# Optimization experiments

Hardware: AMD Instinct MI355X
Metric: run time of the kernel (lower is better)

The kernel has to match this reference:

```python
import jax, jax.numpy as jnp
import numpy as np

B, SP, SH, H = 32, 256, 256, 512
D = 2 * H       # input feature dim (2*hidden_size)
E = H // 2      # per-liner output dim
FD = 4 * H      # fusion linear dim
EPS = 1e-13


def setup_inputs() -> dict:
    key = jax.random.key(0)
    ks = jax.random.split(key, 8)
    s = 0.02
    return dict(
        premise_batch=jax.random.normal(ks[0], (B, SP, D), jnp.float32),
        hypothesis_batch=jax.random.normal(ks[1], (B, SH, D), jnp.float32),
        premise_mask=jax.random.randint(ks[2], (B, SP), 0, 2).astype(jnp.int32),
        hypothesis_mask=jax.random.randint(ks[3], (B, SH), 0, 2).astype(jnp.int32),
        W8=jax.random.normal(ks[4], (8, D, E), jnp.float32) * s,   # liner1..8 weights (in,out)
        B8=jnp.zeros((8, E), jnp.float32),
        Wl=jax.random.normal(ks[5], (8 * E, FD), jnp.float32) * s,  # self.liner
        bl=jnp.zeros((FD,), jnp.float32),
        Wp=jax.random.normal(ks[6], (7 * D, H), jnp.float32) * s,   # self._projection
        bp=jnp.zeros((H,), jnp.float32),
    )


def masked_softmax(logits, mask):
    # ESIM-style: multiply logits by mask, softmax, re-mask, renormalize.
    m = mask[:, None, :]                        # (b,1,kv)
    r = jax.nn.softmax(logits * m, axis=-1) * m
    return r / (r.sum(axis=-1, keepdims=True) + EPS)


def fuse(x, imp_self, imp_inter, W8, B8, Wl, bl):
    # x: (b,s,D); imp_*: (b,s,1). Eight modulated views -> liner1..8 -> concat -> liner+ReLU.
    a1 = imp_self * imp_inter
    a2 = imp_self + imp_inter
    a3 = jnp.maximum(imp_self, imp_inter)
    x1 = x * imp_self
    x2 = x * imp_inter
    mx = jnp.maximum(x1, x2)
    feats = jnp.stack([x * a1, x * a2, x * a3, mx,
                       x * (a1 + 1.0), x * (a2 + 1.0), x * (a3 + 1.0), mx + x], 0)  # (8,b,s,D)
    h = jnp.einsum('kbsd,kde->kbse', feats, W8) + B8[:, None, None, :]              # (8,b,s,E)
    cat = jnp.moveaxis(h, 0, 2).reshape(x.shape[0], x.shape[1], 8 * E)              # concat order 1..8
    return jax.nn.relu(cat @ Wl + bl)           # dropout is identity in eval mode


def reference(premise_batch, hypothesis_batch, premise_mask, hypothesis_mask,
              W8, B8, Wl, bl, Wp, bp):
    pm = premise_mask.astype(jnp.float32)
    hm = hypothesis_mask.astype(jnp.float32)
    scale = 1.0 / jnp.sqrt(jnp.float32(premise_batch.shape[-1]))

    sim = jnp.einsum('bpd,bhd->bph', premise_batch, hypothesis_batch) * scale
    ph = masked_softmax(sim, hm)                               # (b,Sp,Sh)
    hp = masked_softmax(sim.transpose(0, 2, 1), pm)            # (b,Sh,Sp)
    att_p = jnp.einsum('bph,bhd->bpd', ph, hypothesis_batch) * pm[:, :, None]
    att_h = jnp.einsum('bhp,bpd->bhd', hp, premise_batch) * hm[:, :, None]

    sp_attn = jax.nn.softmax(jnp.einsum('bpd,bqd->bpq', premise_batch, premise_batch) * scale, axis=-1)
    sh_attn = jax.nn.softmax(jnp.einsum('bpd,bqd->bpq', hypothesis_batch, hypothesis_batch) * scale, axis=-1)
    self_p = sp_attn @ premise_batch
    self_h = sh_attn @ hypothesis_batch

    imp_p = sp_attn.sum(axis=-2)[..., None]        # (b,Sp,1)
    imp_h = sh_attn.sum(axis=-2)[..., None]        # (b,Sh,1)
    inter_imp_h = ph.sum(axis=-2)[..., None]       # (b,Sh,1)
    inter_imp_p = hp.sum(axis=-2)[..., None]       # (b,Sp,1)

    p_all = fuse(premise_batch, imp_p, inter_imp_p, W8, B8, Wl, bl)
    h_all = fuse(hypothesis_batch, imp_h, inter_imp_h, W8, B8, Wl, bl)

    enh_p = jnp.concatenate([premise_batch, att_p, self_p, p_all,
                             premise_batch * att_p, premise_batch - att_p], axis=-1)
    enh_h = jnp.concatenate([hypothesis_batch, att_h, self_h, h_all,
                             hypothesis_batch * att_h, hypothesis_batch - att_h], axis=-1)
    out_p = jax.nn.relu(enh_p @ Wp + bp)
    out_h = jax.nn.relu(enh_h @ Wp + bp)
    return out_p, out_h
```

## Files before the change

### kernel.cpp

```cpp
#include <hip/hip_runtime.h>
#include <hip/hip_bf16.h>
#include <cmath>

#define BB 32
#define SS 256
#define DD 1024
#define EE 256
#define FDIM 2048
#define HH 512
#define KOUT6 (6 * 1024)
#define NROW (BB * SS)
#define NROW2 (2 * NROW)
#define SIMSZ ((size_t)BB * SS * SS)

static constexpr float SCALE = 1.0f / 32.0f;
static constexpr float EPSF  = 1e-13f;

typedef __attribute__((ext_vector_type(8))) short bf16x8;
typedef __attribute__((ext_vector_type(4))) float f32x4;

__device__ inline float4 ld4(const float* p) { return *(const float4*)p; }
__device__ inline ushort f2b(float f) {
    uint x = __float_as_uint(f);
    x += 0x7fffu + ((x >> 16) & 1u);
    return (ushort)(x >> 16);
}
__device__ inline float b2f(ushort u) { return __uint_as_float(((uint)u) << 16); }
__device__ inline bf16x8 cvt8(const float* v) {
    bf16x8 r;
#pragma unroll
    for (int j = 0; j < 8; ++j) r[j] = (short)f2b(v[j]);
    return r;
}
__device__ inline void b2f8(bf16x8 v, float* o) {
#pragma unroll
    for (int j = 0; j < 8; ++j) o[j] = b2f((ushort)v[j]);
}
__device__ inline bf16x8 ldf8(const float* p) {
    const float4 u0 = ld4(p), u1 = ld4(p + 4);
    float v[8] = {u0.x, u0.y, u0.z, u0.w, u1.x, u1.y, u1.z, u1.w};
    return cvt8(v);
}

typedef __attribute__((address_space(1))) const uchar gas_t;
typedef __attribute__((address_space(3))) uchar las_t;
__device__ inline void gll16(const ushort* g, ushort* l) {
    __builtin_amdgcn_global_load_lds((gas_t*)g, (las_t*)l, 16, 0, 0);
}

__device__ inline int swz_orig_2d() {
    const int n   = blockIdx.y * gridDim.x + blockIdx.x;
    const int tot = gridDim.x * gridDim.y;
    return (n & 7) * (tot >> 3) + (n >> 3);
}
__device__ inline int swz_orig_3d() {
    const int n   = (blockIdx.z * gridDim.y + blockIdx.y) * gridDim.x + blockIdx.x;
    const int tot = gridDim.x * gridDim.y * gridDim.z;
    return (n & 7) * (tot >> 3) + (n >> 3);
}

__global__ __launch_bounds__(256)
void tpose_cvt_k(const float* __restrict__ in, ushort* __restrict__ out,
                 int K, int N, size_t inStride, size_t outStride) {
    __shared__ float T[32][33];
    const float* ib = in  + (size_t)blockIdx.z * inStride;
    ushort*      ob = out + (size_t)blockIdx.z * outStride;
    const int k0 = blockIdx.x * 32, n0 = blockIdx.y * 32;
    const int tx = threadIdx.x & 31, ty = threadIdx.x >> 5;
#pragma unroll
    for (int i = 0; i < 4; ++i) T[ty + 8 * i][tx] = ib[(size_t)(k0 + ty + 8 * i) * N + n0 + tx];
    __syncthreads();
#pragma unroll
    for (int i = 0; i < 4; ++i)
        ob[(size_t)(n0 + ty + 8 * i) * K + k0 + tx] = f2b(T[tx][ty + 8 * i]);
}

__global__ __launch_bounds__(256)
void tpose_wp_k(const float* __restrict__ Wp, ushort* __restrict__ out) {
    __shared__ float T[32][33];
    const int k0 = blockIdx.x * 32, n0 = blockIdx.y * 32;
    const int tx = threadIdx.x & 31, ty = threadIdx.x >> 5;
#pragma unroll
    for (int i = 0; i < 4; ++i) {
        const int k = k0 + ty + 8 * i, n = n0 + tx;
        float v = Wp[(size_t)k * HH + n];
        if (k < DD)           v += Wp[(size_t)(k + 6 * DD) * HH + n];
        else if (k < 2 * DD)  v -= Wp[(size_t)(k + 5 * DD) * HH + n];
        T[ty + 8 * i][tx] = v;
    }
    __syncthreads();
#pragma unroll
    for (int i = 0; i < 4; ++i)
        out[(size_t)(n0 + ty + 8 * i) * KOUT6 + k0 + tx] = f2b(T[tx][ty + 8 * i]);
}

__global__ __launch_bounds__(256)
void prep_xprod_k(const float* __restrict__ P, const float* __restrict__ H,
                  const ushort* __restrict__ attAb,
                  ushort* __restrict__ Xb, ushort* __restrict__ prodb) {
    const int idx = blockIdx.x * 256 + threadIdx.x;
    const int row = idx >> 7, chunk = idx & 127;
    const size_t off = (size_t)row * DD + chunk * 8;
    const float* X = (row < NROW) ? (P + off) : (H + off - (size_t)NROW * DD);
    const float4 x0 = ld4(X), x1 = ld4(X + 4);
    float xv[8] = {x0.x, x0.y, x0.z, x0.w, x1.x, x1.y, x1.z, x1.w};
    float av[8];
    b2f8(*(const bf16x8*)&attAb[off], av);
    float pv[8];
#pragma unroll
    for (int j = 0; j < 8; ++j) pv[j] = xv[j] * av[j];
    *(bf16x8*)&Xb[off]    = cvt8(xv);
    *(bf16x8*)&prodb[off] = cvt8(pv);
}

__global__ __launch_bounds__(256)
void reduce_out_k(float* __restrict__ out, const float* __restrict__ p1,
                  const float* __restrict__ bp) {
    const int gid = blockIdx.x * 256 + threadIdx.x;
    const size_t o = (size_t)gid * 4;
    const float4 a = ld4(&out[o]);
    const float4 b = ld4(&p1[o]);
    const float4 bv = ld4(&bp[(int)(o & 511)]);
    *(float4*)&out[o] = make_float4(fmaxf(a.x + b.x + bv.x, 0.f),
                                    fmaxf(a.y + b.y + bv.y, 0.f),
                                    fmaxf(a.z + b.z + bv.z, 0.f),
                                    fmaxf(a.w + b.w + bv.w, 0.f));
}

__global__ __launch_bounds__(256)
void softmax4_k(ushort* __restrict__ simPH, ushort* __restrict__ simPHT,
                ushort* __restrict__ simPP, ushort* __restrict__ simHH,
                const int* __restrict__ pma, const int* __restrict__ hma) {
    const int job = blockIdx.y;
    ushort* buf = job == 0 ? simPH : job == 1 ? simPHT : job == 2 ? simPP : simHH;
    const int* mask = job == 0 ? hma : job == 1 ? pma : nullptr;
    const int w = threadIdx.x >> 6, lane = threadIdx.x & 63;
    const int row = blockIdx.x * 4 + w;
    const int b = row >> 8;
    ushort* rp = buf + (size_t)row * SS + lane * 4;
    ushort4 u = *(const ushort4*)rp;
    float z[4], mj[4];
    const ushort uv[4] = {u.x, u.y, u.z, u.w};
#pragma unroll
    for (int c = 0; c < 4; ++c) {
        const float v = b2f(uv[c]);
        float m = 1.f;
        if (mask) m = (float)mask[b * SS + lane * 4 + c];
        mj[c] = m; z[c] = v * m;
    }
    float M = fmaxf(fmaxf(z[0], z[1]), fmaxf(z[2], z[3]));
#pragma unroll
    for (int off = 1; off < 64; off <<= 1) M = fmaxf(M, __shfl_xor(M, off));
    float e[4], r[4], sz = 0.f, sr = 0.f;
#pragma unroll
    for (int c = 0; c < 4; ++c) {
        e[c] = expf(z[c] - M);
        r[c] = e[c] * mj[c];
        sz += e[c]; sr += r[c];
    }
#pragma unroll
    for (int off = 1; off < 64; off <<= 1) {
        sz += __shfl_xor(sz, off);
        sr += __shfl_xor(sr, off);
    }
    ushort4 o;
    if (mask) {
        const float d = 1.f / (sr + EPSF * sz);
        o.x = f2b(r[0] * d); o.y = f2b(r[1] * d); o.z = f2b(r[2] * d); o.w = f2b(r[3] * d);
    } else {
        const float d = 1.f / sz;
        o.x = f2b(e[0] * d); o.y = f2b(e[1] * d); o.z = f2b(e[2] * d); o.w = f2b(e[3] * d);
    }
    *(ushort4*)rp = o;
}

__global__ __launch_bounds__(256)
void colsum_p1_k(const ushort* __restrict__ simPP, const ushort* __restrict__ simHH,
                 const ushort* __restrict__ simPHT, const ushort* __restrict__ simPH,
                 float* __restrict__ pbuf) {
    const int job = blockIdx.y, b = blockIdx.x, rc = blockIdx.z, j = threadIdx.x;
    const ushort* src = job == 0 ? simPP : job == 1 ? simHH : job == 2 ? simPHT : simPH;
    const ushort* Mb = src + (size_t)b * SS * SS + (size_t)rc * 32 * SS;
    float s = 0.f;
#pragma unroll 4
    for (int i = 0; i < 32; ++i) s += b2f(Mb[i * SS + j]);
    pbuf[(((size_t)job * BB + b) * 8 + rc) * SS + j] = s;
}

__global__ __launch_bounds__(256)
void colsum_p2_k(const float* __restrict__ pbuf,
                 float* __restrict__ impS, float* __restrict__ impI) {
    const int job = blockIdx.y, b = blockIdx.x, j = threadIdx.x;
    const float* pb = pbuf + ((size_t)job * BB + b) * 8 * SS;
    float s = 0.f;
#pragma unroll
    for (int rc = 0; rc < 8; ++rc) s += pb[rc * SS + j];
    float* dst = job == 0 ? impS : job == 1 ? impS + NROW : job == 2 ? impI : impI + NROW;
    dst[b * SS + j] = s;
}

#define LSWZ(kg, r) ((r) ^ ((kg) << 1))
#define FRAG_R(T, r) (*(const bf16x8*)T[kq][LSWZ(kq, r)])
#define FRAG_G(T, r) (*(const bf16x8*)&T[r][(kq ^ ((r) & 3)) * 8])

#define MFMA_TAIL(afr, bfr)                                                          \
    _Pragma("unroll") for (int m = 0; m < 4; ++m)                                    \
        _Pragma("unroll") for (int n = 0; n < 4; ++n)                                \
            acc[m][n] = __builtin_amdgcn_mfma_f32_16x16x32_bf16(                     \
                afr[m], bfr[n], acc[m][n], 0, 0, 0);

#define MFMA_CORE_R()                                                                \
    {                                                                                \
        bf16x8 afr[4], bfr[4];                                                       \
        _Pragma("unroll") for (int m = 0; m < 4; ++m) afr[m] = FRAG_R(As, wr + m * 16 + fr); \
        _Pragma("unroll") for (int n = 0; n < 4; ++n) bfr[n] = FRAG_R(Bs, wc + n * 16 + fr); \
        MFMA_TAIL(afr, bfr)                                                          \
    }

#define MFMA_CORE_G()                                                                \
    {                                                                                \
        bf16x8 afr[4], bfr[4];                                                       \
        _Pragma("unroll") for (int m = 0; m < 4; ++m) afr[m] = FRAG_G(As, wr + m * 16 + fr); \
        _Pragma("unroll") for (int n = 0; n < 4; ++n) bfr[n] = FRAG_G(Bs, wc + n * 16 + fr); \
        MFMA_TAIL(afr, bfr)                                                          \
    }

#define MFMA_CORE_RG()                                                               \
    {                                                                                \
        bf16x8 afr[4], bfr[4];                                                       \
        _Pragma("unroll") for (int m = 0; m < 4; ++m) afr[m] = FRAG_R(As, wr + m * 16 + fr); \
        _Pragma("unroll") for (int n = 0; n < 4; ++n) bfr[n] = FRAG_G(Bs, wc + n * 16 + fr); \
        MFMA_TAIL(afr, bfr)                                                          \
    }

#define MFMA_PREAMBLE()                                                              \
    const int tid = threadIdx.x;                                                     \
    const int lane = tid & 63;                                                       \
    const int w = tid >> 6;                                                          \
    const int wr = (w >> 1) * 64, wc = (w & 1) * 64;                                 \
    const int fr = lane & 15;                                                        \
    const int kq = lane >> 4;                                                        \
    const int rq = kq * 4;                                                           \
    f32x4 acc[4][4] = {};

#define GLL_STAGE2(seg, pitch, r0, kloc, T)                                          \
    {                                                                                \
        const int rl0_ = w * 32 + (lane >> 2);                                       \
        const int cp_ = lane & 3;                                                    \
        gll16((seg) + (size_t)((r0) + rl0_) * (pitch) + (kloc) + ((cp_ ^ (rl0_ & 3)) * 8), \
              &T[w * 32][0]);                                                        \
        const int rl1_ = rl0_ + 16;                                                  \
        gll16((seg) + (size_t)((r0) + rl1_) * (pitch) + (kloc) + ((cp_ ^ (rl1_ & 3)) * 8), \
              &T[w * 32 + 16][0]);                                                   \
    }

__global__ __launch_bounds__(256)
void mfma_nt_k(const float* __restrict__ P, const float* __restrict__ H,
               ushort* __restrict__ simPH, ushort* __restrict__ simPHT,
               ushort* __restrict__ simPP, ushort* __restrict__ simHH) {
    __shared__ __align__(16) ushort As[4][128][8];
    __shared__ __align__(16) ushort Bs[4][128][8];
    int orig = swz_orig_3d();
    const int cb = orig & 1; orig >>= 1;
    const int rb = orig & 1; orig >>= 1;
    const int g = orig >> 5, b = orig & 31;
    const float* Au = ((g == 2) ? H : P) + (size_t)b * SS * DD;
    const float* Bu = ((g == 1) ? P : H) + (size_t)b * SS * DD;
    const int col0 = cb * 128, row0 = rb * 128;
    MFMA_PREAMBLE();
    for (int k0 = 0; k0 < DD; k0 += 32) {
        bf16x8 ar[2], br[2];
#pragma unroll
        for (int i = 0; i < 2; ++i) {
            const int cid = tid + i * 256, srow = cid >> 2, skc = (cid & 3) * 8;
            ar[i] = ldf8(&Au[(size_t)(row0 + srow) * DD + k0 + skc]);
            br[i] = ldf8(&Bu[(size_t)(col0 + srow) * DD + k0 + skc]);
        }
        __syncthreads();
#pragma unroll
        for (int i = 0; i < 2; ++i) {
            const int cid = tid + i * 256, kg = cid & 3, rr = LSWZ(kg, cid >> 2);
            *(bf16x8*)As[kg][rr] = ar[i];
            *(bf16x8*)Bs[kg][rr] = br[i];
        }
        __syncthreads();
        MFMA_CORE_R();
    }
    ushort* Cb = (g == 0 ? simPH : g == 1 ? simPP : simHH) + (size_t)b * SS * SS;
#pragma unroll
    for (int m = 0; m < 4; ++m)
#pragma unroll
        for (int n = 0; n < 4; ++n) {
            const int c = col0 + wc + n * 16 + fr;
            const int r0 = row0 + wr + m * 16 + rq;
#pragma unroll
            for (int r = 0; r < 4; ++r) Cb[(size_t)(r0 + r) * SS + c] = f2b(acc[m][n][r] * SCALE);
            if (g == 0) {
                ushort* Tb = simPHT + (size_t)b * SS * SS;
                ushort4 t;
                t.x = f2b(acc[m][n][0] * SCALE); t.y = f2b(acc[m][n][1] * SCALE);
                t.z = f2b(acc[m][n][2] * SCALE); t.w = f2b(acc[m][n][3] * SCALE);
                *(ushort4*)&Tb[(size_t)c * SS + r0] = t;
            }
        }
}

__global__ __launch_bounds__(256)
void mfma_att_k(const ushort* __restrict__ ph, const ushort* __restrict__ hp,
                const ushort* __restrict__ spA, const ushort* __restrict__ shA,
                const ushort* __restrict__ PbT, const ushort* __restrict__ HbT,
                const int* __restrict__ pma, const int* __restrict__ hma,
                ushort* __restrict__ attAb, ushort* __restrict__ selfAb) {
    __shared__ __align__(16) ushort As[128][32];
    __shared__ __align__(16) ushort Bs[128][32];
    int orig = swz_orig_3d();
    const int x = orig & 7; orig >>= 3;
    const int y = orig & 1; orig >>= 1;
    const int g = orig >> 5, b = orig & 31;
    const ushort* W  = (g == 0 ? ph : g == 1 ? hp : g == 2 ? spA : shA) + (size_t)b * SS * SS;
    const ushort* BT = ((g == 0 || g == 3) ? HbT : PbT) + (size_t)b * DD * SS;
    const int* rmask = g == 0 ? pma + b * SS : g == 1 ? hma + b * SS : nullptr;
    const int side = (g == 1 || g == 3);
    ushort* Ob = (g < 2 ? attAb : selfAb) + ((size_t)side * NROW + (size_t)b * SS) * DD;
    const int col0 = x * 128, row0 = y * 128;
    MFMA_PREAMBLE();
    for (int k0 = 0; k0 < SS; k0 += 32) {
        __syncthreads();
        GLL_STAGE2(W,  SS, row0, k0, As);
        GLL_STAGE2(BT, SS, col0, k0, Bs);
        __syncthreads();
        MFMA_CORE_G();
    }
#pragma unroll
    for (int m = 0; m < 4; ++m)
#pragma unroll
        for (int n = 0; n < 4; ++n) {
            const int c = col0 + wc + n * 16 + fr;
#pragma unroll
            for (int r = 0; r < 4; ++r) {
                const int rr = row0 + wr + m * 16 + rq + r;
                const float mm = rmask ? (float)rmask[rr] : 1.0f;
                Ob[(size_t)rr * DD + c] = f2b(acc[m][n][r] * mm);
            }
        }
}

__global__ __launch_bounds__(256)
void mfma_fuse_k(const float* __restrict__ P, const float* __restrict__ H,
                 const float* __restrict__ impS, const float* __restrict__ impI,
                 const ushort* __restrict__ W8T, const float* __restrict__ B8v,
                 ushort* __restrict__ catb) {
    __shared__ __align__(16) ushort As[4][128][8];
    __shared__ __align__(16) ushort Bs[128][32];
    const int orig = swz_orig_2d();
    const int cb = orig & 15, rb = orig >> 4;
    const int kf = cb >> 1, e0 = (cb & 1) * 128, row0 = rb * 128;
    const float* X = (row0 < NROW) ? P : H;
    const int rbase = (row0 < NROW) ? row0 : row0 - NROW;
    MFMA_PREAMBLE();
    const ushort* Wk = W8T + (size_t)kf * EE * DD;

    int srow_[2]; float sA[2], iA[2], cf[2];
#pragma unroll
    for (int i = 0; i < 2; ++i) {
        const int cid = tid + i * 256;
        srow_[i] = cid >> 2;
        const float s_ = impS[row0 + srow_[i]], i_ = impI[row0 + srow_[i]];
        sA[i] = s_; iA[i] = i_;
        float c = 0.f;
        switch (kf) {
            case 0: c = s_ * i_;             break;
            case 1: c = s_ + i_;             break;
            case 2: c = fmaxf(s_, i_);       break;
            case 4: c = s_ * i_ + 1.f;       break;
            case 5: c = s_ + i_ + 1.f;       break;
            case 6: c = fmaxf(s_, i_) + 1.f; break;
            default: break;
        }
        cf[i] = c;
    }
    for (int k0 = 0; k0 < DD; k0 += 32) {
        bf16x8 ar[2];
#pragma unroll
        for (int i = 0; i < 2; ++i) {
            const int cid = tid + i * 256, skc = (cid & 3) * 8;
            const float* src = &X[(size_t)(rbase + srow_[i]) * DD + k0 + skc];
            const float4 u0 = ld4(src), u1 = ld4(src + 4);
            float v[8] = {u0.x, u0.y, u0.z, u0.w, u1.x, u1.y, u1.z, u1.w};
            if (kf == 3) {
#pragma unroll
                for (int j = 0; j < 8; ++j) v[j] = fmaxf(v[j] * sA[i], v[j] * iA[i]);
            } else if (kf == 7) {
#pragma unroll
                for (int j = 0; j < 8; ++j) v[j] = fmaxf(v[j] * sA[i], v[j] * iA[i]) + v[j];
            } else {
#pragma unroll
                for (int j = 0; j < 8; ++j) v[j] *= cf[i];
            }
            ar[i] = cvt8(v);
        }
        __syncthreads();
        GLL_STAGE2(Wk, DD, e0, k0, Bs);
#pragma unroll
        for (int i = 0; i < 2; ++i) {
            const int cid = tid + i * 256, kg = cid & 3, rr = LSWZ(kg, cid >> 2);
            *(bf16x8*)As[kg][rr] = ar[i];
        }
        __syncthreads();
        MFMA_CORE_RG();
    }
#pragma unroll
    for (int m = 0; m < 4; ++m)
#pragma unroll
        for (int n = 0; n < 4; ++n) {
            const int el = e0 + wc + n * 16 + fr;
            const float bv = B8v[kf * EE + el];
#pragma unroll
            for (int r = 0; r < 4; ++r) {
                const int rr = row0 + wr + m * 16 + rq + r;
                catb[(size_t)rr * FDIM + kf * EE + el] = f2b(acc[m][n][r] + bv);
            }
        }
}

__global__ __launch_bounds__(256)
void mfma_lin_k(const ushort* __restrict__ A, const ushort* __restrict__ BT,
                const float* __restrict__ bias, ushort* __restrict__ C) {
    __shared__ __align__(16) ushort As[128][32];
    __shared__ __align__(16) ushort Bs[128][32];
    const int orig = swz_orig_2d();
    const int col0 = (orig & 15) * 128, row0 = (orig >> 4) * 128;
    MFMA_PREAMBLE();
    for (int k0 = 0; k0 < FDIM; k0 += 32) {
        __syncthreads();
        GLL_STAGE2(A,  FDIM, row0, k0, As);
        GLL_STAGE2(BT, FDIM, col0, k0, Bs);
        __syncthreads();
        MFMA_CORE_G();
    }
#pragma unroll
    for (int m = 0; m < 4; ++m)
#pragma unroll
        for (int n = 0; n < 4; ++n) {
            const int c = col0 + wc + n * 16 + fr;
            const float bv = bias[c];
#pragma unroll
            for (int r = 0; r < 4; ++r) {
                const int rr = row0 + wr + m * 16 + rq + r;
                C[(size_t)rr * FDIM + c] = f2b(fmaxf(acc[m][n][r] + bv, 0.f));
            }
        }
}

__device__ inline void out_seg(int k0, const ushort* Xb, const ushort* attAb,
                               const ushort* selfAb, const ushort* pallb,
                               const ushort* prodb,
                               const ushort*& seg, int& pitch, int& kloc) {
    switch (k0 >> 10) {
        case 0:  seg = Xb;     pitch = DD;   kloc = k0;          break;
        case 1:  seg = attAb;  pitch = DD;   kloc = k0 - DD;     break;
        case 2:  seg = selfAb; pitch = DD;   kloc = k0 - 2 * DD; break;
        case 3:
        case 4:  seg = pallb;  pitch = FDIM; kloc = k0 - 3 * DD; break;
        default: seg = prodb;  pitch = DD;   kloc = k0 - 5 * DD; break;
    }
}

__global__ __launch_bounds__(256)
void mfma_out_k(const ushort* __restrict__ Xb, const ushort* __restrict__ attAb,
                const ushort* __restrict__ selfAb, const ushort* __restrict__ pallb,
                const ushort* __restrict__ prodb, const ushort* __restrict__ WpT,
                const float* __restrict__ bp, float* __restrict__ dst0,
                float* __restrict__ dst1, int kchunk, int finalize) {
    __shared__ __align__(16) ushort As[128][32];
    __shared__ __align__(16) ushort Bs[128][32];
    int orig = swz_orig_3d();
    const int x = orig & 3; orig >>= 2;
    const int y = orig & 127; orig >>= 7;
    const int z = orig;
    const int col0 = x * 128, row0 = y * 128;
    const int kbase = z * kchunk;
    float* dst = z == 0 ? dst0 : dst1;
    MFMA_PREAMBLE();
    for (int t = 0; t < kchunk / 32; ++t) {
        const int k0 = kbase + t * 32;
        const ushort* seg; int pitch, kloc;
        out_seg(k0, Xb, attAb, selfAb, pallb, prodb, seg, pitch, kloc);
        __syncthreads();
        GLL_STAGE2(seg, pitch, row0, kloc, As);
        GLL_STAGE2(WpT, KOUT6, col0, k0, Bs);
        __syncthreads();
        MFMA_CORE_G();
    }
#pragma unroll
    for (int m = 0; m < 4; ++m)
#pragma unroll
        for (int n = 0; n < 4; ++n) {
            const int c = col0 + wc + n * 16 + fr;
            const float bv = finalize ? bp[c] : 0.f;
#pragma unroll
            for (int r = 0; r < 4; ++r) {
                const int rr = row0 + wr + m * 16 + rq + r;
                const float v = acc[m][n][r] + bv;
                dst[(size_t)rr * HH + c] = finalize ? fmaxf(v, 0.f) : v;
            }
        }
}

extern "C" void kernel_launch(void* const* d_in, const int* in_sizes, int n_in,
                              void* d_out, int out_size, void* d_ws, size_t ws_size,
                              hipStream_t stream) {
    const float* P   = (const float*)d_in[0];
    const float* Hb  = (const float*)d_in[1];
    const int*   pma = (const int*)d_in[2];
    const int*   hma = (const int*)d_in[3];
    const float* W8  = (const float*)d_in[4];
    const float* B8v = (const float*)d_in[5];
    const float* Wl  = (const float*)d_in[6];
    const float* bl  = (const float*)d_in[7];
    const float* Wp  = (const float*)d_in[8];
    const float* bp  = (const float*)d_in[9];

    char* base = (char*)d_ws;
    ushort* simPH  = (ushort*)base;
    ushort* simPHT = simPH  + SIMSZ;
    ushort* simPP  = simPHT + SIMSZ;
    ushort* simHH  = simPP  + SIMSZ;
    ushort* PbT    = simHH + SIMSZ;
    ushort* HbT    = PbT + (size_t)NROW * DD;
    ushort* catb   = (ushort*)base;
    ushort* Xb     = (ushort*)base;
    ushort* prodb  = Xb + (size_t)NROW2 * DD;
    char* cur = base + (size_t)NROW2 * FDIM * 2;
    auto alloc_f = [&](size_t n) { float*  p = (float*)cur;  cur += n * 4; return p; };
    auto alloc_u = [&](size_t n) { ushort* p = (ushort*)cur; cur += n * 2; return p; };
    float*  impS   = alloc_f(NROW2);
    float*  impI   = alloc_f(NROW2);
    ushort* attAb  = alloc_u((size_t)NROW2 * DD);
    ushort* selfAb = alloc_u((size_t)NROW2 * DD);
    ushort* pallb  = alloc_u((size_t)NROW2 * FDIM);
    ushort* WlT    = alloc_u((size_t)FDIM * FDIM);
    ushort* WpT    = alloc_u((size_t)HH * KOUT6);
    ushort* W8T    = alloc_u((size_t)8 * EE * DD);
    float*  pbuf   = alloc_f((size_t)4 * BB * 8 * SS);
    float*  part1  = alloc_f((size_t)NROW2 * HH);

    const size_t need_split = (size_t)((char*)(part1 + (size_t)NROW2 * HH) - base);
    const bool split = ws_size >= need_split;

    float* outp = (float*)d_out;
    const dim3 blk(256);

    tpose_cvt_k<<<dim3(8, 32, BB), blk, 0, stream>>>(P,  PbT, SS, DD, (size_t)SS * DD, (size_t)DD * SS);
    tpose_cvt_k<<<dim3(8, 32, BB), blk, 0, stream>>>(Hb, HbT, SS, DD, (size_t)SS * DD, (size_t)DD * SS);
    tpose_cvt_k<<<dim3(FDIM / 32, FDIM / 32, 1), blk, 0, stream>>>(Wl, WlT, FDIM, FDIM, 0, 0);
    tpose_wp_k<<<dim3(KOUT6 / 32, HH / 32, 1), blk, 0, stream>>>(Wp, WpT);
    tpose_cvt_k<<<dim3(DD / 32, EE / 32, 8), blk, 0, stream>>>(W8, W8T, DD, EE,
                                                               (size_t)DD * EE, (size_t)EE * DD);

    mfma_nt_k<<<dim3(2, 2, 96), blk, 0, stream>>>(P, Hb, simPH, simPHT, simPP, simHH);
    softmax4_k<<<dim3(NROW / 4, 4), blk, 0, stream>>>(simPH, simPHT, simPP, simHH, pma, hma);
    colsum_p1_k<<<dim3(BB, 4, 8), blk, 0, stream>>>(simPP, simHH, simPHT, simPH, pbuf);
    colsum_p2_k<<<dim3(BB, 4), blk, 0, stream>>>(pbuf, impS, impI);
    mfma_att_k<<<dim3(8, 2, 128), blk, 0, stream>>>(simPH, simPHT, simPP, simHH, PbT, HbT,
                                                    pma, hma, attAb, selfAb);

    mfma_fuse_k<<<dim3(16, 128), blk, 0, stream>>>(P, Hb, impS, impI, W8T, B8v, catb);
    mfma_lin_k<<<dim3(16, 128), blk, 0, stream>>>(catb, WlT, bl, pallb);
    prep_xprod_k<<<dim3(NROW2 * DD / 8 / 256), blk, 0, stream>>>(P, Hb, attAb, Xb, prodb);
    if (split) {
        mfma_out_k<<<dim3(4, 128, 2), blk, 0, stream>>>(Xb, attAb, selfAb, pallb, prodb,
                                                        WpT, bp, outp, part1, KOUT6 / 2, 0);
        reduce_out_k<<<dim3(NROW2 * HH / 4 / 256), blk, 0, stream>>>(outp, part1, bp);
    } else {
        mfma_out_k<<<dim3(4, 128, 1), blk, 0, stream>>>(Xb, attAb, selfAb, pallb, prodb,
                                                        WpT, bp, outp, outp, KOUT6, 1);
    }

    (void)in_sizes; (void)n_in; (void)out_size; (void)ws_size;
}
```

Baseline: 716.9 us.

## Factor per-row scale out of fuse GEMM and precompute bf16 inputs

Six of the eight modulated views are x times a per-row scalar, so the fuse GEMM now multiplies unscaled bf16 x by the weights and applies the coefficient in the epilogue. The two max-based views are rewritten as smin*x + (smax-smin)*relu(x), which needs a second accumulator fed by a sign-masked copy of x. A separate conversion kernel writes bf16 x once so the GEMM tiles can stream it with direct global-to-LDS loads. This trades an extra launch and an extra buffer pass against removing per-tile fp32 loads and elementwise scaling. It also changes rounding, since scaling now happens after the bf16 product, and it changes the LDS swizzle signature.

```diff
diff --git a/kernel.cpp b/kernel.cpp
--- a/kernel.cpp
+++ b/kernel.cpp
@@ -92,6 +92,18 @@
 #pragma unroll
     for (int i = 0; i < 4; ++i)
         out[(size_t)(n0 + ty + 8 * i) * KOUT6 + k0 + tx] = f2b(T[tx][ty + 8 * i]);
+}
+
+__global__ __launch_bounds__(256)
+void cvt_xb_k(const float* __restrict__ P, const float* __restrict__ H,
+              ushort* __restrict__ Xb) {
+    const int idx = blockIdx.x * 256 + threadIdx.x;
+    const int row = idx >> 7, chunk = idx & 127;
+    const size_t off = (size_t)row * DD + chunk * 8;
+    const float* X = (row < NROW) ? (P + off) : (H + off - (size_t)NROW * DD);
+    const float4 x0 = ld4(X), x1 = ld4(X + 4);
+    float xv[8] = {x0.x, x0.y, x0.z, x0.w, x1.x, x1.y, x1.z, x1.w};
+    *(bf16x8*)&Xb[off] = cvt8(xv);
 }
 
 __global__ __launch_bounds__(256)
@@ -200,21 +212,22 @@
 }
 
 #define LSWZ(kg, r) ((r) ^ ((kg) << 1))
+#define SIG(r) (((r) >> 1) & 3)
 #define FRAG_R(T, r) (*(const bf16x8*)T[kq][LSWZ(kq, r)])
-#define FRAG_G(T, r) (*(const bf16x8*)&T[r][(kq ^ ((r) & 3)) * 8])
-
-#define MFMA_TAIL(afr, bfr)                                                          \
+#define FRAG_G(T, r) (*(const bf16x8*)&T[r][(kq ^ SIG(r)) * 8])
+
+#define MFMA_TAIL(afr, bfr, ac)                                                      \
     _Pragma("unroll") for (int m = 0; m < 4; ++m)                                    \
         _Pragma("unroll") for (int n = 0; n < 4; ++n)                                \
-            acc[m][n] = __builtin_amdgcn_mfma_f32_16x16x32_bf16(                     \
-                afr[m], bfr[n], acc[m][n], 0, 0, 0);
+            ac[m][n] = __builtin_amdgcn_mfma_f32_16x16x32_bf16(                      \
+                afr[m], bfr[n], ac[m][n], 0, 0, 0);
 
 #define MFMA_CORE_R()                                                                \
     {                                                                                \
         bf16x8 afr[4], bfr[4];                                                       \
         _Pragma("unroll") for (int m = 0; m < 4; ++m) afr[m] = FRAG_R(As, wr + m * 16 + fr); \
         _Pragma("unroll") for (int n = 0; n < 4; ++n) bfr[n] = FRAG_R(Bs, wc + n * 16 + fr); \
-        MFMA_TAIL(afr, bfr)                                                          \
+        MFMA_TAIL(afr, bfr, acc)                                                     \
     }
 
 #define MFMA_CORE_G()                                                                \
@@ -222,15 +235,7 @@
         bf16x8 afr[4], bfr[4];                                                       \
         _Pragma("unroll") for (int m = 0; m < 4; ++m) afr[m] = FRAG_G(As, wr + m * 16 + fr); \
         _Pragma("unroll") for (int n = 0; n < 4; ++n) bfr[n] = FRAG_G(Bs, wc + n * 16 + fr); \
-        MFMA_TAIL(afr, bfr)                                                          \
-    }
-
-#define MFMA_CORE_RG()                                                               \
-    {                                                                                \
-        bf16x8 afr[4], bfr[4];                                                       \
-        _Pragma("unroll") for (int m = 0; m < 4; ++m) afr[m] = FRAG_R(As, wr + m * 16 + fr); \
-        _Pragma("unroll") for (int n = 0; n < 4; ++n) bfr[n] = FRAG_G(Bs, wc + n * 16 + fr); \
-        MFMA_TAIL(afr, bfr)                                                          \
+        MFMA_TAIL(afr, bfr, acc)                                                     \
     }
 
 #define MFMA_PREAMBLE()                                                              \
@@ -247,10 +252,10 @@
     {                                                                                \
         const int rl0_ = w * 32 + (lane >> 2);                                       \
         const int cp_ = lane & 3;                                                    \
-        gll16((seg) + (size_t)((r0) + rl0_) * (pitch) + (kloc) + ((cp_ ^ (rl0_ & 3)) * 8), \
+        gll16((seg) + (size_t)((r0) + rl0_) * (pitch) + (kloc) + ((cp_ ^ SIG(rl0_)) * 8), \
               &T[w * 32][0]);                                                        \
         const int rl1_ = rl0_ + 16;                                                  \
-        gll16((seg) + (size_t)((r0) + rl1_) * (pitch) + (kloc) + ((cp_ ^ (rl1_ & 3)) * 8), \
+        gll16((seg) + (size_t)((r0) + rl1_) * (pitch) + (kloc) + ((cp_ ^ SIG(rl1_)) * 8), \
               &T[w * 32 + 16][0]);                                                   \
     }
 
@@ -346,68 +351,24 @@
 }
 
 __global__ __launch_bounds__(256)
-void mfma_fuse_k(const float* __restrict__ P, const float* __restrict__ H,
-                 const float* __restrict__ impS, const float* __restrict__ impI,
-                 const ushort* __restrict__ W8T, const float* __restrict__ B8v,
-                 ushort* __restrict__ catb) {
-    __shared__ __align__(16) ushort As[4][128][8];
+void mfma_fuse_pure_k(const ushort* __restrict__ Xb, const float* __restrict__ impS,
+                      const float* __restrict__ impI, const ushort* __restrict__ W8T,
+                      const float* __restrict__ B8v, ushort* __restrict__ catb) {
+    __shared__ __align__(16) ushort As[128][32];
     __shared__ __align__(16) ushort Bs[128][32];
     const int orig = swz_orig_2d();
-    const int cb = orig & 15, rb = orig >> 4;
-    const int kf = cb >> 1, e0 = (cb & 1) * 128, row0 = rb * 128;
-    const float* X = (row0 < NROW) ? P : H;
-    const int rbase = (row0 < NROW) ? row0 : row0 - NROW;
+    const int cb = orig % 12, rb = orig / 12;
+    const int kidx = cb >> 1;
+    const int kf = kidx + (kidx >= 3 ? 1 : 0);
+    const int e0 = (cb & 1) * 128, row0 = rb * 128;
     MFMA_PREAMBLE();
     const ushort* Wk = W8T + (size_t)kf * EE * DD;
-
-    int srow_[2]; float sA[2], iA[2], cf[2];
-#pragma unroll
-    for (int i = 0; i < 2; ++i) {
-        const int cid = tid + i * 256;
-        srow_[i] = cid >> 2;
-        const float s_ = impS[row0 + srow_[i]], i_ = impI[row0 + srow_[i]];
-        sA[i] = s_; iA[i] = i_;
-        float c = 0.f;
-        switch (kf) {
-            case 0: c = s_ * i_;             break;
-            case 1: c = s_ + i_;             break;
-            case 2: c = fmaxf(s_, i_);       break;
-            case 4: c = s_ * i_ + 1.f;       break;
-            case 5: c = s_ + i_ + 1.f;       break;
-            case 6: c = fmaxf(s_, i_) + 1.f; break;
-            default: break;
-        }
-        cf[i] = c;
-    }
     for (int k0 = 0; k0 < DD; k0 += 32) {
-        bf16x8 ar[2];
-#pragma unroll
-        for (int i = 0; i < 2; ++i) {
-            const int cid = tid + i * 256, skc = (cid & 3) * 8;
-            const float* src = &X[(size_t)(rbase + srow_[i]) * DD + k0 + skc];
-            const float4 u0 = ld4(src), u1 = ld4(src + 4);
-            float v[8] = {u0.x, u0.y, u0.z, u0.w, u1.x, u1.y, u1.z, u1.w};
-            if (kf == 3) {
-#pragma unroll
-                for (int j = 0; j < 8; ++j) v[j] = fmaxf(v[j] * sA[i], v[j] * iA[i]);
-            } else if (kf == 7) {
-#pragma unroll
-                for (int j = 0; j < 8; ++j) v[j] = fmaxf(v[j] * sA[i], v[j] * iA[i]) + v[j];
-            } else {
-#pragma unroll
-                for (int j = 0; j < 8; ++j) v[j] *= cf[i];
-            }
-            ar[i] = cvt8(v);
-        }
-        __syncthreads();
+        __syncthreads();
+        GLL_STAGE2(Xb, DD, row0, k0, As);
         GLL_STAGE2(Wk, DD, e0, k0, Bs);
-#pragma unroll
-        for (int i = 0; i < 2; ++i) {
-            const int cid = tid + i * 256, kg = cid & 3, rr = LSWZ(kg, cid >> 2);
-            *(bf16x8*)As[kg][rr] = ar[i];
-        }
-        __syncthreads();
-        MFMA_CORE_RG();
+        __syncthreads();
+        MFMA_CORE_G();
     }
 #pragma unroll
     for (int m = 0; m < 4; ++m)
@@ -417,8 +378,84 @@
             const float bv = B8v[kf * EE + el];
 #pragma unroll
             for (int r = 0; r < 4; ++r) {
-                const int rr = row0 + wr + m * 16 + rq + r;
-                catb[(size_t)rr * FDIM + kf * EE + el] = f2b(acc[m][n][r] + bv);
+                const int row = row0 + wr + m * 16 + rq + r;
+                const float s_ = impS[row], i_ = impI[row];
+                float coef;
+                switch (kf) {
+                    case 0: coef = s_ * i_;             break;
+                    case 1: coef = s_ + i_;             break;
+                    case 2: coef = fmaxf(s_, i_);       break;
+                    case 4: coef = s_ * i_ + 1.f;       break;
+                    case 5: coef = s_ + i_ + 1.f;       break;
+                    default: coef = fmaxf(s_, i_) + 1.f; break;
+                }
+                catb[(size_t)row * FDIM + kf * EE + el] = f2b(coef * acc[m][n][r] + bv);
+            }
+        }
+}
+
+__global__ __launch_bounds__(256)
+void mfma_fuse_dual_k(const ushort* __restrict__ Xb, const float* __restrict__ impS,
+                      const float* __restrict__ impI, const ushort* __restrict__ W8T,
+                      const float* __restrict__ B8v, ushort* __restrict__ catb) {
+    __shared__ __align__(16) ushort AsX[4][128][8];
+    __shared__ __align__(16) ushort AsP[4][128][8];
+    __shared__ __align__(16) ushort Bs[128][32];
+    const int orig = swz_orig_2d();
+    const int cb = orig & 3, rb = orig >> 2;
+    const int kf = (cb >> 1) ? 7 : 3;
+    const int e0 = (cb & 1) * 128, row0 = rb * 128;
+    MFMA_PREAMBLE();
+    f32x4 accP[4][4] = {};
+    const ushort* Wk = W8T + (size_t)kf * EE * DD;
+    for (int k0 = 0; k0 < DD; k0 += 32) {
+        bf16x8 xr[2], pr[2];
+#pragma unroll
+        for (int i = 0; i < 2; ++i) {
+            const int cid = tid + i * 256, srow = cid >> 2, skc = (cid & 3) * 8;
+            xr[i] = *(const bf16x8*)&Xb[(size_t)(row0 + srow) * DD + k0 + skc];
+#pragma unroll
+            for (int j = 0; j < 8; ++j) {
+                const short s = xr[i][j];
+                pr[i][j] = (s & (short)0x8000) ? (short)0 : s;
+            }
+        }
+        __syncthreads();
+        GLL_STAGE2(Wk, DD, e0, k0, Bs);
+#pragma unroll
+        for (int i = 0; i < 2; ++i) {
+            const int cid = tid + i * 256, kg = cid & 3, rr = LSWZ(kg, cid >> 2);
+            *(bf16x8*)AsX[kg][rr] = xr[i];
+            *(bf16x8*)AsP[kg][rr] = pr[i];
+        }
+        __syncthreads();
+        {
+            bf16x8 ax[4], ap[4], bfr[4];
+#pragma unroll
+            for (int m = 0; m < 4; ++m) {
+                ax[m] = FRAG_R(AsX, wr + m * 16 + fr);
+                ap[m] = FRAG_R(AsP, wr + m * 16 + fr);
+            }
+#pragma unroll
+            for (int n = 0; n < 4; ++n) bfr[n] = FRAG_G(Bs, wc + n * 16 + fr);
+            MFMA_TAIL(ax, bfr, acc)
+            MFMA_TAIL(ap, bfr, accP)
+        }
+    }
+#pragma unroll
+    for (int m = 0; m < 4; ++m)
+#pragma unroll
+        for (int n = 0; n < 4; ++n) {
+            const int el = e0 + wc + n * 16 + fr;
+            const float bv = B8v[kf * EE + el];
+#pragma unroll
+            for (int r = 0; r < 4; ++r) {
+                const int row = row0 + wr + m * 16 + rq + r;
+                const float s_ = impS[row], i_ = impI[row];
+                const float smax = fmaxf(s_, i_), smin = fminf(s_, i_);
+                const float gg = (kf == 3) ? smin : smin + 1.f;
+                catb[(size_t)row * FDIM + kf * EE + el] =
+                    f2b((smax - smin) * accP[m][n][r] + gg * acc[m][n][r] + bv);
             }
         }
 }
@@ -545,6 +582,8 @@
     float*  pbuf   = alloc_f((size_t)4 * BB * 8 * SS);
     float*  part1  = alloc_f((size_t)NROW2 * HH);
 
+    ushort* XbE = pallb;
+
     const size_t need_split = (size_t)((char*)(part1 + (size_t)NROW2 * HH) - base);
     const bool split = ws_size >= need_split;
 
@@ -565,7 +604,9 @@
     mfma_att_k<<<dim3(8, 2, 128), blk, 0, stream>>>(simPH, simPHT, simPP, simHH, PbT, HbT,
                                                     pma, hma, attAb, selfAb);
 
-    mfma_fuse_k<<<dim3(16, 128), blk, 0, stream>>>(P, Hb, impS, impI, W8T, B8v, catb);
+    cvt_xb_k<<<dim3(NROW2 * DD / 8 / 256), blk, 0, stream>>>(P, Hb, XbE);
+    mfma_fuse_pure_k<<<dim3(12, 128), blk, 0, stream>>>(XbE, impS, impI, W8T, B8v, catb);
+    mfma_fuse_dual_k<<<dim3(4, 128), blk, 0, stream>>>(XbE, impS, impI, W8T, B8v, catb);
     mfma_lin_k<<<dim3(16, 128), blk, 0, stream>>>(catb, WlT, bl, pallb);
     prep_xprod_k<<<dim3(NROW2 * DD / 8 / 256), blk, 0, stream>>>(P, Hb, attAb, Xb, prodb);
     if (split) {
```

New measurement: 688.8 us. 3.9% less time.
